# Kernel optimization log

Hardware: AMD Instinct MI355X
Metric: run time of the kernel (lower is better)

## Reference

```python
import jax, jax.numpy as jnp
import numpy as np
import math

EPS = 1e-5
N_HEADS = 4


def _ln(x, g, b):
    mu = jnp.mean(x, axis=-1, keepdims=True)
    var = jnp.mean((x - mu) ** 2, axis=-1, keepdims=True)
    return (x - mu) * jax.lax.rsqrt(var + EPS) * g + b


def _eq_ln(s, v, g, b, vscale):
    # scalar LayerNorm + equivariant vector norm rescaling
    s = _ln(s, g, b)
    vn = jnp.sqrt(jnp.sum(v * v, axis=-1, keepdims=True))  # (B,N,C,1)
    v = v / (vn + EPS) * jnp.mean(vn, axis=-2, keepdims=True) * vscale[None, None, :, None]
    return s, v


def _block(s, v, pos, Wq, bq, Wk, bk, Wv, bv, Wo, bo, w_dist, b_dist, Wvv, Wvo,
           g1, be1, vs1, g2, be2, vs2, Wf1, bf1, Wf2, bf2, Wfv1, Wfv2):
    B, N, S = s.shape
    D = S // N_HEADS
    # --- norm1 + attention ---
    sn, vn = _eq_ln(s, v, g1, be1, vs1)
    q = (sn @ Wq + bq).reshape(B, N, N_HEADS, D)
    k = (sn @ Wk + bk).reshape(B, N, N_HEADS, D)
    vs = (sn @ Wv + bv).reshape(B, N, N_HEADS, D)
    attn = jnp.einsum('bnhd,bmhd->bhnm', q, k) / math.sqrt(D)
    # pairwise Euclidean distance via the |x|^2 + |y|^2 - 2xy trick (clamped for sqrt safety)
    p2 = jnp.sum(pos * pos, axis=-1)  # (B,N)
    d2 = p2[:, :, None] + p2[:, None, :] - 2.0 * jnp.einsum('bnd,bmd->bnm', pos, pos)
    dist = jnp.sqrt(jnp.maximum(d2, 1e-12))  # (B,N,N)
    # dist_proj: Linear(1 -> n_heads) + Softplus, applied per pair
    bias = jax.nn.softplus(dist[..., None] * w_dist + b_dist)  # (B,N,N,H)
    attn = jax.nn.softmax(attn - jnp.transpose(bias, (0, 3, 1, 2)), axis=-1)  # (B,H,N,N)
    attn_mean = jnp.mean(attn, axis=1)  # (B,N,N)
    s_attn = jnp.einsum('bhnm,bmhd->bnhd', attn, vs).reshape(B, N, S) @ Wo + bo
    # vector channel mixing + rotation by head-averaged attention
    v_mix = jnp.einsum('bncx,ce->bnex', vn, Wvv)          # (B,N,C,3)
    v_attn = jnp.einsum('bnm,bmcx->bncx', attn_mean, v_mix)
    v_attn = jnp.einsum('bncx,ce->bnex', v_attn, Wvo)
    s = s + s_attn
    v = v + v_attn
    # --- norm2 + FFN ---
    sn, vn = _eq_ln(s, v, g2, be2, vs2)
    s = s + (jax.nn.gelu(sn @ Wf1 + bf1, approximate=False) @ Wf2 + bf2)
    v = v + jnp.einsum('bnhx,hc->bncx', jnp.einsum('bncx,ch->bnhx', vn, Wfv1), Wfv2)
    return s, v


def setup_inputs() -> dict:
    B, N, S, C, H = 4, 2048, 256, 64, N_HEADS
    key = jax.random.key(0)
    ks = jax.random.split(key, 24)

    def nrm(k, shape, scale=0.02):
        return jax.random.normal(k, shape, dtype=jnp.float32) * scale

    return {
        's': jax.random.normal(ks[0], (B, N, S), dtype=jnp.float32),
        'v': jax.random.normal(ks[1], (B, N, C, 3), dtype=jnp.float32),
        'pos': jax.random.normal(ks[2], (B, N, 3), dtype=jnp.float32),
        'Wq': nrm(ks[3], (S, S)), 'bq': nrm(ks[4], (S,)),
        'Wk': nrm(ks[5], (S, S)), 'bk': nrm(ks[6], (S,)),
        'Wv': nrm(ks[7], (S, S)), 'bv': nrm(ks[8], (S,)),
        'Wo': nrm(ks[9], (S, S)), 'bo': nrm(ks[10], (S,)),
        'w_dist': nrm(ks[11], (H,), 0.5), 'b_dist': nrm(ks[12], (H,), 0.5),
        'Wvv': nrm(ks[13], (C, C)), 'Wvo': nrm(ks[14], (C, C)),
        'g1': jnp.ones((S,), jnp.float32), 'be1': jnp.zeros((S,), jnp.float32),
        'vs1': jnp.ones((C,), jnp.float32),
        'g2': jnp.ones((S,), jnp.float32), 'be2': jnp.zeros((S,), jnp.float32),
        'vs2': jnp.ones((C,), jnp.float32),
        'Wf1': nrm(ks[15], (S, 4 * S)), 'bf1': nrm(ks[16], (4 * S,)),
        'Wf2': nrm(ks[17], (4 * S, S)), 'bf2': nrm(ks[18], (S,)),
        'Wfv1': nrm(ks[19], (C, 4 * C)), 'Wfv2': nrm(ks[20], (4 * C, C)),
    }


def reference(s, v, pos, Wq, bq, Wk, bk, Wv, bv, Wo, bo, w_dist, b_dist, Wvv, Wvo,
              g1, be1, vs1, g2, be2, vs2, Wf1, bf1, Wf2, bf2, Wfv1, Wfv2):
    return _block(s, v, pos, Wq, bq, Wk, bk, Wv, bv, Wo, bo, w_dist, b_dist, Wvv, Wvo,
                  g1, be1, vs1, g2, be2, vs2, Wf1, bf1, Wf2, bf2, Wfv1, Wfv2)
```

## Files before the change

kernel.cpp:

```cpp
#include <hip/hip_runtime.h>
#include <hip/hip_bf16.h>

using bf16 = __hip_bfloat16;
typedef __attribute__((ext_vector_type(8))) short short8;
typedef __attribute__((ext_vector_type(4))) float float4v;
typedef __attribute__((ext_vector_type(16))) float f32x16;
typedef __attribute__((ext_vector_type(4))) unsigned uint4v;

__device__ __forceinline__ float b2f(bf16 x){ return __bfloat162float(x); }
__device__ __forceinline__ bf16  f2b(float x){ return __float2bfloat16(x); }
__device__ __forceinline__ bf16  tob(float x){ return f2b(x); }
__device__ __forceinline__ bf16  tob(bf16 x){ return x; }
__device__ __forceinline__ float frcp(float x){ return __builtin_amdgcn_rcpf(x); }
__device__ __forceinline__ float bs2f(short s){
  unsigned u = ((unsigned)(unsigned short)s) << 16;
  return __builtin_bit_cast(float, u);
}
__device__ __forceinline__ unsigned cvt_pk_bf16(float lo, float hi){
  unsigned r; asm("v_cvt_pk_bf16_f32 %0, %1, %2" : "=v"(r) : "v"(lo), "v"(hi)); return r;
}
__device__ __forceinline__ void plswap(unsigned &a, unsigned &b){
  asm("v_permlane32_swap_b32 %0, %1" : "+v"(a), "+v"(b));
}

#define EPSV 1e-5f
#define Z16 {0.f,0.f,0.f,0.f,0.f,0.f,0.f,0.f,0.f,0.f,0.f,0.f,0.f,0.f,0.f,0.f}

__global__ __launch_bounds__(256) void pos_kernel(const float* __restrict__ pos,
                                                  float* __restrict__ posf, int rows){
  int r = blockIdx.x*256 + threadIdx.x;
  if (r >= rows) return;
  float x = pos[3*r], y = pos[3*r+1], z = pos[3*r+2];
  posf[4*r] = x; posf[4*r+1] = y; posf[4*r+2] = z; posf[4*r+3] = x*x + y*y + z*z;
}

struct WTDesc { const float* src; bf16* dst; int rows, cols; };
struct WTPack { WTDesc d[10]; };

__global__ __launch_bounds__(256) void wtrans_kernel(WTPack p){
  WTDesc w = p.d[blockIdx.z];
  long r0 = (long)blockIdx.y*32, c0 = (long)blockIdx.x*32;
  if (r0 >= w.rows || c0 >= w.cols) return;
  __shared__ bf16 tile[32][33];
  int tx = threadIdx.x & 31, ty = threadIdx.x >> 5;
#pragma unroll
  for (int i = ty; i < 32; i += 8) tile[i][tx] = f2b(w.src[(r0+i)*w.cols + c0 + tx]);
  __syncthreads();
#pragma unroll
  for (int i = ty; i < 32; i += 8) w.dst[(c0+i)*w.rows + r0 + tx] = tile[tx][i];
}

template<typename TI>
__global__ __launch_bounds__(256) void transpose_kernel(
    const TI* __restrict__ in, long ldin, long is1, long is2,
    bf16* __restrict__ out, long ldout, long os1, long os2, int Z2)
{
  int z = blockIdx.z, z1 = z / Z2, z2 = z - z1*Z2;
  in  += (long)z1*is1 + (long)z2*is2;
  out += (long)z1*os1 + (long)z2*os2;
  __shared__ bf16 tile[32][33];
  int tx = threadIdx.x & 31, ty = threadIdx.x >> 5;
  long r0 = (long)blockIdx.y*32, c0 = (long)blockIdx.x*32;
#pragma unroll
  for (int i = ty; i < 32; i += 8) tile[i][tx] = tob(in[(r0+i)*ldin + c0 + tx]);
  __syncthreads();
#pragma unroll
  for (int i = ty; i < 32; i += 8) out[(c0+i)*ldout + r0 + tx] = tile[tx][i];
}

__global__ __launch_bounds__(256) void bcat_kernel(const float* __restrict__ bq,
                                                   const float* __restrict__ bk,
                                                   const float* __restrict__ bv,
                                                   float* __restrict__ bqkv,
                                                   float* __restrict__ kmax){
  int j = blockIdx.x*256 + threadIdx.x;
  if (blockIdx.x == 0 && threadIdx.x < 16) kmax[threadIdx.x] = 0.f;
  if (j >= 768) return;
  bqkv[j] = (j < 256) ? bq[j] : (j < 512) ? bk[j-256] : bv[j-512];
}

__global__ __launch_bounds__(256) void ln_kernel(const float* __restrict__ x,
                                                 const float* __restrict__ g,
                                                 const float* __restrict__ be,
                                                 bf16* __restrict__ out){
  const long row = blockIdx.x;
  const int t = threadIdx.x;
  __shared__ float r1[256], r2[256];
  float v = x[(row<<8) + t];
  r1[t] = v; r2[t] = v*v; __syncthreads();
  for (int s=128;s>0;s>>=1){
    if (t<s){ r1[t] += r1[t+s]; r2[t] += r2[t+s]; }
    __syncthreads();
  }
  const float mu = r1[0] * (1.f/256.f);
  const float var = r2[0] * (1.f/256.f) - mu*mu;
  const float rstd = rsqrtf(fmaxf(var, 0.f) + EPSV);
  out[(row<<8)+t] = f2b((v-mu)*rstd*g[t] + be[t]);
}

__global__ __launch_bounds__(192) void vnorm1_kernel(const float* __restrict__ vin,
                                                     const float* __restrict__ vs1,
                                                     bf16* __restrict__ vnX){
  const long row = blockIdx.x;
  const int t = threadIdx.x;
  __shared__ float vv[192], nrm[64];
  __shared__ float smean;
  vv[t] = vin[row*192 + t];
  __syncthreads();
  if (t < 64){
    float a = vv[3*t], b = vv[3*t+1], c = vv[3*t+2];
    nrm[t] = sqrtf(a*a + b*b + c*c);
  }
  __syncthreads();
  if (t == 0){ float s = 0.f; for (int i=0;i<64;i++) s += nrm[i]; smean = s*(1.f/64.f); }
  __syncthreads();
  const int c = t/3, x = t - 3*c;
  const float val = vv[t] / (nrm[c] + EPSV) * smean * vs1[c];
  vnX[row*192 + x*64 + c] = f2b(val);
}

__global__ __launch_bounds__(192) void vnorm2_kernel(const float* __restrict__ v2X,
                                                     const float* __restrict__ vs2,
                                                     bf16* __restrict__ vn2X){
  const long row = blockIdx.x;
  const int t = threadIdx.x;
  __shared__ float vv[192], nrm[64];
  __shared__ float smean;
  vv[t] = v2X[row*192 + t];
  __syncthreads();
  if (t < 64){
    float a = vv[t], b = vv[t+64], c = vv[t+128];
    nrm[t] = sqrtf(a*a + b*b + c*c);
  }
  __syncthreads();
  if (t == 0){ float s = 0.f; for (int i=0;i<64;i++) s += nrm[i]; smean = s*(1.f/64.f); }
  __syncthreads();
  const int c = t & 63;
  vn2X[row*192 + t] = f2b(vv[t] / (nrm[c] + EPSV) * smean * vs2[c]);
}

__global__ __launch_bounds__(256) void knorm_kernel(const bf16* __restrict__ qkv,
                                                    float* __restrict__ kmax){
  const int bh = blockIdx.x, b = bh>>2, h = bh&3;
  const int t = threadIdx.x;
  __shared__ float red[256];
  long row = (long)b*2048 + (long)blockIdx.y*256 + t;
  const short8* kp = (const short8*)(qkv + row*768 + 256 + h*64);
  float ss = 0.f;
#pragma unroll
  for (int c=0;c<8;c++){
    short8 v = kp[c];
#pragma unroll
    for (int j=0;j<8;j++){ float f = bs2f(v[j]); ss = fmaf(f,f,ss); }
  }
  red[t] = ss; __syncthreads();
  for (int s=128;s>0;s>>=1){ if (t<s) red[t] = fmaxf(red[t], red[t+s]); __syncthreads(); }
  if (t==0) atomicMax((unsigned*)&kmax[bh], __float_as_uint(red[0]));
}

#define ATT_K_OFF   0
#define ATT_V_OFF   4096
#define ATT_X_OFF   9216
#define ATT_P_OFF   24576
#define ATT_TILE    25088
#define ATT_GRP     50176
#define ATT_LACC    98304
#define ATT_SMEM    100352

__global__ __launch_bounds__(512, 2) void attn_kernel(
    const bf16* __restrict__ qkv,
    const bf16* __restrict__ vsT,
    const bf16* __restrict__ vmixT,
    const float* __restrict__ posf,
    const float* __restrict__ kmaxA,
    const float* __restrict__ w_dist, const float* __restrict__ b_dist,
    bf16* __restrict__ sA,
    bf16* __restrict__ slab)
{
  __shared__ __align__(16) char smem[ATT_SMEM];
  const int qb = blockIdx.x;
  const int bh = blockIdx.y;
  const int b  = bh >> 2, h = bh & 3;
  const int tid = threadIdx.x;
  const int w = tid >> 6, lane = tid & 63;
  const int g = w >> 2, qw = w & 3;
  const int lq = lane & 31, hi = lane >> 5;
  const int gtid = tid & 255;

  const int qloc = qb*128 + qw*32 + lq;
  const long rowQ = (long)b*2048 + qloc;

  short8 qf[4];
  {
    const bf16* qp = qkv + rowQ*768 + h*64 + hi*8;
#pragma unroll
    for (int kc=0;kc<4;kc++) qf[kc] = *(const short8*)(qp + kc*16);
  }
  float q2 = 0.f;
#pragma unroll
  for (int kc=0;kc<4;kc++)
#pragma unroll
    for (int j=0;j<8;j++){ float qv = bs2f(qf[kc][j]); q2 = fmaf(qv,qv,q2); }
  q2 += __shfl_xor(q2, 32);
  const float mxs = sqrtf(q2 * kmaxA[bh]) * 0.125f;
  const float wh = w_dist[h], bhd = b_dist[h];
  const float4v pn = *(const float4v*)(posf + (long)b*8192 + (long)qloc*4);
  const float m2x = -2.f*pn[0], m2y = -2.f*pn[1], m2z = -2.f*pn[2], pnw = pn[3];

  f32x16 O[2]  = {Z16, Z16};
  f32x16 VM[6] = {Z16, Z16, Z16, Z16, Z16, Z16};
  float lacc = 0.f;

  short8 stK, stV, stX0, stX1, stX2; float4v stP;
  const int sm = gtid >> 3, sc = gtid & 7;
  const int vd = gtid >> 2, vc = gtid & 3;
  const bf16* Kg = qkv + (long)b*2048*768 + 256 + h*64;
  const bf16* Vg = vsT + (long)b*524288 + (long)h*131072;
  const bf16* Xg = vmixT + (long)b*393216;
  const float* Pg = posf + (long)b*8192;
  char* gbase = smem + g*ATT_GRP;

  auto LOADT = [&](int m0){
    stK  = *(const short8*)(Kg + (long)(m0+sm)*768 + sc*8);
    stV  = *(const short8*)(Vg + (long)vd*2048 + m0 + vc*8);
    stX0 = *(const short8*)(Xg + (long)vd*2048 + m0 + vc*8);
    stX1 = *(const short8*)(Xg + (long)(64+vd)*2048 + m0 + vc*8);
    stX2 = *(const short8*)(Xg + (long)(128+vd)*2048 + m0 + vc*8);
    if (gtid < 32) stP = *(const float4v*)(Pg + (long)(m0+gtid)*4);
  };
  auto WRITET = [&](char* buf){
    *(short8*)(buf + ATT_K_OFF + sm*128 + ((sc ^ (sm&7))<<4)) = stK;
    *(short8*)(buf + ATT_V_OFF + vd*80 + vc*16) = stV;
    *(short8*)(buf + ATT_X_OFF + vd*80 + vc*16) = stX0;
    *(short8*)(buf + ATT_X_OFF + (64+vd)*80 + vc*16) = stX1;
    *(short8*)(buf + ATT_X_OFF + (128+vd)*80 + vc*16) = stX2;
    if (gtid < 32) *(float4v*)(buf + ATT_P_OFF + gtid*16) = stP;
  };

  auto COMPUTE = [&](const char* buf){
    const char* Kb = buf + ATT_K_OFF;
    const char* Vb = buf + ATT_V_OFF;
    const char* Xb = buf + ATT_X_OFF;
    const float4v* pmb = (const float4v*)(buf + ATT_P_OFF);
    f32x16 S = Z16;
#pragma unroll
    for (int kc=0;kc<4;kc++){
      short8 kf = *(const short8*)(Kb + lq*128 + (((kc*2+hi) ^ (lq&7))<<4));
      S = __builtin_amdgcn_mfma_f32_32x32x16_bf16(kf, qf[kc], S, 0, 0, 0);
    }
    float P[16];
#pragma unroll
    for (int gg=0; gg<4; gg++){
#pragma unroll
      for (int i=0;i<4;i++){
        float4v pm = pmb[gg*8 + hi*4 + i];
        float d2 = fmaf(m2x, pm[0], fmaf(m2y, pm[1], fmaf(m2z, pm[2], pnw + pm[3])));
        float dist = sqrtf(fmaxf(d2, 1e-12f));
        float sig = frcp(1.f + __expf(fmaf(dist, wh, bhd)));
        float p = __expf(fmaf(S[gg*4+i], 0.125f, -mxs)) * sig;
        lacc += p;
        P[gg*4+i] = p;
      }
    }
    unsigned pk[8];
#pragma unroll
    for (int t=0;t<8;t++) pk[t] = cvt_pk_bf16(P[2*t], P[2*t+1]);
    plswap(pk[0], pk[2]); plswap(pk[1], pk[3]);
    plswap(pk[4], pk[6]); plswap(pk[5], pk[7]);
    uint4v y0v = {pk[0], pk[1], pk[2], pk[3]};
    uint4v y1v = {pk[4], pk[5], pk[6], pk[7]};
    short8 Y0 = __builtin_bit_cast(short8, y0v);
    short8 Y1 = __builtin_bit_cast(short8, y1v);
#pragma unroll
    for (int dblk=0; dblk<2; dblk++){
      short8 v0 = *(const short8*)(Vb + (dblk*32+lq)*80 + hi*16);
      short8 v1 = *(const short8*)(Vb + (dblk*32+lq)*80 + 32 + hi*16);
      O[dblk] = __builtin_amdgcn_mfma_f32_32x32x16_bf16(v0, Y0, O[dblk], 0,0,0);
      O[dblk] = __builtin_amdgcn_mfma_f32_32x32x16_bf16(v1, Y1, O[dblk], 0,0,0);
    }
#pragma unroll
    for (int eblk=0; eblk<6; eblk++){
      short8 x0 = *(const short8*)(Xb + (eblk*32+lq)*80 + hi*16);
      short8 x1 = *(const short8*)(Xb + (eblk*32+lq)*80 + 32 + hi*16);
      VM[eblk] = __builtin_amdgcn_mfma_f32_32x32x16_bf16(x0, Y0, VM[eblk], 0,0,0);
      VM[eblk] = __builtin_amdgcn_mfma_f32_32x32x16_bf16(x1, Y1, VM[eblk], 0,0,0);
    }
  };

  LOADT(g*32);
  WRITET(gbase);
  __syncthreads();
#pragma unroll 1
  for (int i=0; i<32; ++i){
    if (i < 31) LOADT((2*(i+1)+g)*32);
    COMPUTE(gbase + (i&1)*ATT_TILE);
    if (i < 31) WRITET(gbase + ((i+1)&1)*ATT_TILE);
    __syncthreads();
  }

  float* laccT = (float*)(smem + ATT_LACC);
  laccT[w*64 + lane] = lacc;
  if (g == 1){
    float* Od = (float*)(smem + ATT_GRP) + (qw*64+lane)*33;
#pragma unroll
    for (int r=0;r<16;r++){ Od[r] = O[0][r]; Od[16+r] = O[1][r]; }
  }
  __syncthreads();
  const float lsum = laccT[qw*64+lq] + laccT[qw*64+32+lq]
                   + laccT[(4+qw)*64+lq] + laccT[(4+qw)*64+32+lq];
  if (g == 0){
    const float* Od = (const float*)(smem + ATT_GRP) + (qw*64+lane)*33;
#pragma unroll
    for (int r=0;r<16;r++){ O[0][r] += Od[r]; O[1][r] += Od[16+r]; }
  }
  __syncthreads();
#pragma unroll
  for (int hf=0; hf<2; hf++){
    if (g == 0){
      float* Vd = (float*)smem + (qw*64+lane)*49;
#pragma unroll
      for (int e=0;e<3;e++)
#pragma unroll
        for (int r=0;r<16;r++) Vd[e*16+r] = VM[hf*3+e][r];
    }
    __syncthreads();
    if (g == 1){
      const float* Vd = (const float*)smem + (qw*64+lane)*49;
#pragma unroll
      for (int e=0;e<3;e++)
#pragma unroll
        for (int r=0;r<16;r++) VM[hf*3+e][r] += Vd[e*16+r];
    }
    __syncthreads();
  }

  const float sinv = frcp(lsum);
  if (g == 0){
    char* scr = smem + qw*12544;
#pragma unroll
    for (int dblk=0; dblk<2; dblk++)
#pragma unroll
      for (int pp=0; pp<8; pp++){
        const int r = 2*pp;
        const int d = dblk*32 + (r&3) + 8*(r>>2) + 4*hi;
        unsigned u = cvt_pk_bf16(O[dblk][r]*sinv, O[dblk][r+1]*sinv);
        *(unsigned*)(scr + lq*136 + d*2) = u;
      }
  } else {
    const float vinv = 0.25f * sinv;
    char* scr = smem + ATT_GRP + qw*12544;
#pragma unroll
    for (int eblk=0; eblk<6; eblk++)
#pragma unroll
      for (int pp=0; pp<8; pp++){
        const int r = 2*pp;
        const int e = eblk*32 + (r&3) + 8*(r>>2) + 4*hi;
        unsigned u = cvt_pk_bf16(VM[eblk][r]*vinv, VM[eblk][r+1]*vinv);
        *(unsigned*)(scr + lq*392 + e*2) = u;
      }
  }
  __syncthreads();
  if (g == 0){
    const char* scr = smem + qw*12544;
    const int q = lane >> 1, half = lane & 1;
    const char* src = scr + q*136 + half*64;
    char* dst = (char*)(sA + (long)(b*2048 + qb*128 + qw*32 + q)*256 + h*64 + half*32);
#pragma unroll
    for (int i=0;i<8;i++)
      *(unsigned long long*)(dst + i*8) = *(const unsigned long long*)(src + i*8);
  } else {
    const char* scr = smem + ATT_GRP + qw*12544;
    const int q = lane >> 1, half = lane & 1;
    const char* src = scr + q*392 + half*192;
    char* dst = (char*)(slab + (long)h*1572864
                        + (long)(b*2048 + qb*128 + qw*32 + q)*192 + half*96);
#pragma unroll
    for (int i=0;i<24;i++)
      *(unsigned long long*)(dst + i*8) = *(const unsigned long long*)(src + i*8);
  }
}

__global__ __launch_bounds__(256) void hred_kernel(const bf16* __restrict__ slab,
                                                   bf16* __restrict__ out){
  long i = (long)blockIdx.x*256 + threadIdx.x;
  if (i >= 196608) return;
  const short8* s0 = (const short8*)slab + i;
  short8 a = s0[0], b = s0[196608], c = s0[2*196608], d = s0[3*196608];
  short8 o;
#pragma unroll
  for (int j=0;j<8;j++){
    float f = bs2f(a[j]) + bs2f(b[j]) + bs2f(c[j]) + bs2f(d[j]);
    bf16 hv = f2b(f); o[j] = *(short*)&hv;
  }
  ((short8*)out)[i] = o;
}

template<int ACT, int OUTM>
__global__ __launch_bounds__(256) void tgemm_kernel(
    const bf16* __restrict__ A, long lda,
    const bf16* __restrict__ BT, long ldb,
    const float* __restrict__ bias,
    const float* __restrict__ resid,
    void* __restrict__ Cv, long ldc,
    int K)
{
  __shared__ __align__(16) bf16 As[2][128*32];
  __shared__ __align__(16) bf16 Bs[2][128*32];
  const int tid = threadIdx.x;
  const int w = tid >> 6, lane = tid & 63;
  const int wr = w >> 1, wc = w & 1;
  const int col = lane & 15, quad = lane >> 4;
  const long rowA0 = (long)blockIdx.y*128;
  const long colB0 = (long)blockIdx.x*128;

  const int tr = tid >> 2, tc = tid & 3;
  const bf16* Ag = A + (rowA0 + tr)*lda + tc*8;
  const bf16* Bg = BT + (colB0 + tr)*ldb + tc*8;

  short8 sa[2], sb[2];
  auto LOAD = [&](int k0){
#pragma unroll
    for (int c=0;c<2;c++){
      sa[c] = *(const short8*)(Ag + (long)c*64*lda + k0);
      sb[c] = *(const short8*)(Bg + (long)c*64*ldb + k0);
    }
  };
  auto STORE = [&](int buf){
#pragma unroll
    for (int c=0;c<2;c++){
      *(short8*)(&As[buf][(tr + 64*c)*32 + tc*8]) = sa[c];
      *(short8*)(&Bs[buf][(tr + 64*c)*32 + tc*8]) = sb[c];
    }
  };

  float4v acc[4][4];
#pragma unroll
  for (int m=0;m<4;m++)
#pragma unroll
    for (int n=0;n<4;n++) acc[m][n] = (float4v){0.f,0.f,0.f,0.f};

  LOAD(0); STORE(0);
  __syncthreads();
  const int nk = K >> 5;
#pragma unroll 1
  for (int ks=0; ks<nk; ++ks){
    if (ks+1 < nk) LOAD((ks+1)*32);
    const bf16* Ab = &As[ks&1][(wr*64 + col)*32 + quad*8];
    const bf16* Bb = &Bs[ks&1][(wc*64 + col)*32 + quad*8];
    short8 af[4], bfv[4];
#pragma unroll
    for (int m=0;m<4;m++) af[m] = *(const short8*)(Ab + m*16*32);
#pragma unroll
    for (int n=0;n<4;n++) bfv[n] = *(const short8*)(Bb + n*16*32);
#pragma unroll
    for (int m=0;m<4;m++)
#pragma unroll
      for (int n=0;n<4;n++)
        acc[m][n] = __builtin_amdgcn_mfma_f32_16x16x32_bf16(af[m], bfv[n], acc[m][n], 0, 0, 0);
    if (ks+1 < nk) STORE((ks+1)&1);
    __syncthreads();
  }

#pragma unroll
  for (int m=0;m<4;m++){
    const long ci0 = rowA0 + wr*64 + m*16 + quad*4;
#pragma unroll
    for (int n=0;n<4;n++){
      const long cj = colB0 + wc*64 + n*16 + col;
      const float bbias = bias ? bias[cj] : 0.f;
#pragma unroll
      for (int r=0;r<4;r++){
        const long ci = ci0 + r;
        float val = acc[m][n][r] + bbias;
        if (ACT == 1) val = 0.5f*val*(1.f + erff(val*0.70710678118654752f));
        if (resid) val += resid[ci*ldc + cj];
        if (OUTM == 0) ((bf16*)Cv)[ci*ldc + cj] = f2b(val);
        else           ((float*)Cv)[ci*ldc + cj] = val;
      }
    }
  }
}

template<int MT, int NT, int ACT, int OUTM, int RXIL, int CXIL>
__global__ __launch_bounds__(64) void gemm_kernel(
    const bf16* __restrict__ A, long lda, long As1, long As2,
    const bf16* __restrict__ BT, long ldb, long Bs1, long Bs2,
    const float* __restrict__ bias,
    const float* __restrict__ resid, long ldr, long Rs1, long Rs2,
    void* __restrict__ Cv, long ldc, long Cs1, long Cs2,
    int K, int Z2, int KS)
{
  int z = blockIdx.z;
  int zz = z / KS, ks = z - zz*KS;
  int z1 = zz / Z2, z2 = zz - z1*Z2;
  A  += (long)z1*As1 + (long)z2*As2 + (long)ks*K;
  BT += (long)z1*Bs1 + (long)z2*Bs2 + (long)ks*K;
  if (resid) resid += (long)z1*Rs1 + (long)z2*Rs2;
  const long cbase = (long)z1*Cs1 + (long)z2*Cs2;

  const int lane = threadIdx.x;
  const int col = lane & 15, quad = lane >> 4;
  const long rowA0 = (long)blockIdx.y*(16*MT);
  const long colB0 = (long)blockIdx.x*(16*NT);

  float4v acc[MT][NT];
#pragma unroll
  for (int m=0;m<MT;m++)
#pragma unroll
    for (int n=0;n<NT;n++) acc[m][n] = (float4v){0.f,0.f,0.f,0.f};

  const bf16* ap[MT];
  const bf16* bp[NT];
#pragma unroll
  for (int m=0;m<MT;m++) ap[m] = A + (rowA0 + m*16 + col)*lda + quad*8;
#pragma unroll
  for (int n=0;n<NT;n++) bp[n] = BT + (colB0 + n*16 + col)*ldb + quad*8;

  for (int k0 = 0; k0 < K; k0 += 32){
    short8 a[MT], bb[NT];
#pragma unroll
    for (int m=0;m<MT;m++){ a[m] = *(const short8*)ap[m]; ap[m] += 32; }
#pragma unroll
    for (int n=0;n<NT;n++){ bb[n] = *(const short8*)bp[n]; bp[n] += 32; }
#pragma unroll
    for (int m=0;m<MT;m++)
#pragma unroll
      for (int n=0;n<NT;n++)
        acc[m][n] = __builtin_amdgcn_mfma_f32_16x16x32_bf16(a[m], bb[n], acc[m][n], 0, 0, 0);
  }

#pragma unroll
  for (int m=0;m<MT;m++){
    const long ri = rowA0 + m*16 + quad*4;
#pragma unroll
    for (int n=0;n<NT;n++){
      const long cj = colB0 + n*16 + col;
      const float bbias = bias ? bias[cj] : 0.f;
#pragma unroll
      for (int r=0;r<4;r++){
        const long ci = ri + r;
        float val = acc[m][n][r] + bbias;
        if (ACT == 1) val = 0.5f*val*(1.f + erff(val*0.70710678118654752f));
        if (resid){
          const long raddr = RXIL ? ((ci/3)*192 + cj*3 + (ci%3)) : (ci*ldr + cj);
          val += resid[raddr];
        }
        const long caddr = CXIL ? (cbase + (ci/3)*192 + cj*3 + (ci%3))
                                : (cbase + ci*ldc + cj);
        if (OUTM == 0)      ((bf16*)Cv)[caddr] = f2b(val);
        else if (OUTM == 1) ((float*)Cv)[caddr] = val;
        else                unsafeAtomicAdd(&((float*)Cv)[caddr], val);
      }
    }
  }
}

extern "C" void kernel_launch(void* const* d_in, const int* in_sizes, int n_in,
                              void* d_out, int out_size, void* d_ws, size_t ws_size,
                              hipStream_t stream)
{
  const float* s    = (const float*)d_in[0];
  const float* v    = (const float*)d_in[1];
  const float* pos  = (const float*)d_in[2];
  const float* Wq   = (const float*)d_in[3];
  const float* bq   = (const float*)d_in[4];
  const float* Wk   = (const float*)d_in[5];
  const float* bk   = (const float*)d_in[6];
  const float* Wv   = (const float*)d_in[7];
  const float* bv   = (const float*)d_in[8];
  const float* Wo   = (const float*)d_in[9];
  const float* bo   = (const float*)d_in[10];
  const float* w_d  = (const float*)d_in[11];
  const float* b_d  = (const float*)d_in[12];
  const float* Wvv  = (const float*)d_in[13];
  const float* Wvo  = (const float*)d_in[14];
  const float* g1   = (const float*)d_in[15];
  const float* be1  = (const float*)d_in[16];
  const float* vs1  = (const float*)d_in[17];
  const float* g2   = (const float*)d_in[18];
  const float* be2  = (const float*)d_in[19];
  const float* vs2  = (const float*)d_in[20];
  const float* Wf1  = (const float*)d_in[21];
  const float* bf1  = (const float*)d_in[22];
  const float* Wf2  = (const float*)d_in[23];
  const float* bf2  = (const float*)d_in[24];
  const float* Wfv1 = (const float*)d_in[25];
  const float* Wfv2 = (const float*)d_in[26];

  float* outS = (float*)d_out;
  float* outV = outS + (size_t)4*2048*256;

  char* w = (char*)d_ws;
  size_t o = 0;
  auto alloc = [&](size_t bytes)->char* {
    char* p = w + o;
    o = (o + bytes + 255) & ~(size_t)255;
    return p;
  };
  float* posf  = (float*)alloc(131072);
  bf16* WqkvT = (bf16*)alloc(393216);
  bf16* WoT   = (bf16*)alloc(131072);
  bf16* Wf1T  = (bf16*)alloc(524288);
  bf16* Wf2T  = (bf16*)alloc(524288);
  bf16* WvvT  = (bf16*)alloc(8192);
  bf16* WvoT  = (bf16*)alloc(8192);
  bf16* Wfv1T = (bf16*)alloc(32768);
  bf16* Wfv2T = (bf16*)alloc(32768);
  float* bqkv = (float*)alloc(3072);
  float* kmax = (float*)alloc(64);
  bf16* sn    = (bf16*)alloc(4194304);
  bf16* qkv   = (bf16*)alloc(12582912);
  bf16* vsT   = (bf16*)alloc(4194304);
  bf16* sA    = (bf16*)alloc(4194304);
  float* s2   = (float*)alloc(8388608);
  bf16* vnX   = (bf16*)alloc(3145728);
  bf16* vmixX = (bf16*)alloc(3145728);
  bf16* vmixXT= (bf16*)alloc(3145728);
  float* v2X  = (float*)alloc(6291456);
  bf16* slab  = (bf16*)alloc(12582912);
  bf16* h1    = (bf16*)alloc(16777216);
  bf16* vn2X  = vnX;
  bf16* tvXb  = vmixX;
  bf16* hv    = qkv;
  if (o > ws_size) return;

  pos_kernel<<<32, 256, 0, stream>>>(pos, posf, 8192);
  WTPack pk;
  pk.d[0] = {Wq,   WqkvT,          256, 256};
  pk.d[1] = {Wk,   WqkvT + 65536,  256, 256};
  pk.d[2] = {Wv,   WqkvT + 131072, 256, 256};
  pk.d[3] = {Wo,   WoT,            256, 256};
  pk.d[4] = {Wf1,  Wf1T,           256, 1024};
  pk.d[5] = {Wf2,  Wf2T,           1024, 256};
  pk.d[6] = {Wvv,  WvvT,           64, 64};
  pk.d[7] = {Wvo,  WvoT,           64, 64};
  pk.d[8] = {Wfv1, Wfv1T,          64, 256};
  pk.d[9] = {Wfv2, Wfv2T,          256, 64};
  wtrans_kernel<<<dim3(32,32,10), 256, 0, stream>>>(pk);
  bcat_kernel<<<3, 256, 0, stream>>>(bq, bk, bv, bqkv, kmax);

  ln_kernel<<<8192, 256, 0, stream>>>(s, g1, be1, sn);
  vnorm1_kernel<<<8192, 192, 0, stream>>>(v, vs1, vnX);

  gemm_kernel<2,4,0,0,0,0><<<dim3(1,768,1), 64, 0, stream>>>(vnX,64,0,0, WvvT,64,0,0,
      nullptr, nullptr,0,0,0, vmixX,64,0,0, 64, 1, 1);
  transpose_kernel<bf16><<<dim3(6,64,4), 256, 0, stream>>>(vmixX, 192, 393216,0,
      vmixXT, 2048, 393216,0, 1);

  tgemm_kernel<0,0><<<dim3(6,64), 256, 0, stream>>>(sn,256, WqkvT,256,
      bqkv, nullptr, qkv,768, 256);
  transpose_kernel<bf16><<<dim3(2,64,16), 256, 0, stream>>>(qkv+512, 768, 1572864,64,
      vsT, 2048, 524288,131072, 4);

  knorm_kernel<<<dim3(16,8), 256, 0, stream>>>(qkv, kmax);
  attn_kernel<<<dim3(16,16), 512, 0, stream>>>(qkv, vsT, vmixXT, posf, kmax,
      w_d, b_d, sA, slab);
  hred_kernel<<<768, 256, 0, stream>>>(slab, tvXb);

  tgemm_kernel<0,1><<<dim3(2,64), 256, 0, stream>>>(sA,256, WoT,256,
      bo, s, s2,256, 256);

  gemm_kernel<2,4,0,1,1,0><<<dim3(1,768,1), 64, 0, stream>>>(tvXb,64,0,0, WvoT,64,0,0,
      nullptr, v,0,0,0, v2X,64,0,0, 64, 1, 1);

  ln_kernel<<<8192, 256, 0, stream>>>(s2, g2, be2, sn);
  tgemm_kernel<1,0><<<dim3(8,64), 256, 0, stream>>>(sn,256, Wf1T,256,
      bf1, nullptr, h1,1024, 256);
  tgemm_kernel<0,1><<<dim3(2,64), 256, 0, stream>>>(h1,1024, Wf2T,1024,
      bf2, s2, outS,256, 1024);

  vnorm2_kernel<<<8192, 192, 0, stream>>>(v2X, vs2, vn2X);
  gemm_kernel<2,4,0,0,0,0><<<dim3(4,768,1), 64, 0, stream>>>(vn2X,64,0,0, Wfv1T,64,0,0,
      nullptr, nullptr,0,0,0, hv,256,0,0, 64, 1, 1);
  gemm_kernel<2,4,0,1,0,1><<<dim3(1,768,1), 64, 0, stream>>>(hv,256,0,0, Wfv2T,256,0,0,
      nullptr, v2X,64,0,0, outV,0,0,0, 256, 1, 1);
}
```

Before: 403.2 us.

## Use wave-shuffle reductions and 64-row GEMM tiles, route Wfv1 through tiled GEMM

Replaces the shared-memory tree reductions in the layernorm, vector-norm and key-norm kernels with wavefront xor-shuffle reductions, which removes most barriers. Shrinks the tiled GEMM from 128x128 to 64x128 block tiles, doubling the grid so more blocks are in flight for these mid-sized matrices. Also moves the vector FFN first projection from the small 64-thread gemm onto the tiled kernel. Smaller tiles reuse less data per block and add more launch overhead in exchange for better occupancy.

```diff
diff --git a/kernel.cpp b/kernel.cpp
--- a/kernel.cpp
+++ b/kernel.cpp
@@ -84,16 +84,21 @@
                                                  const float* __restrict__ be,
                                                  bf16* __restrict__ out){
   const long row = blockIdx.x;
-  const int t = threadIdx.x;
-  __shared__ float r1[256], r2[256];
+  const int t = threadIdx.x, lane = t & 63, wv = t >> 6;
+  __shared__ float ws1[4], ws2[4];
   float v = x[(row<<8) + t];
-  r1[t] = v; r2[t] = v*v; __syncthreads();
-  for (int s=128;s>0;s>>=1){
-    if (t<s){ r1[t] += r1[t+s]; r2[t] += r2[t+s]; }
-    __syncthreads();
-  }
-  const float mu = r1[0] * (1.f/256.f);
-  const float var = r2[0] * (1.f/256.f) - mu*mu;
+  float s1 = v, s2 = v*v;
+#pragma unroll
+  for (int off=32; off; off>>=1){
+    s1 += __shfl_xor(s1, off);
+    s2 += __shfl_xor(s2, off);
+  }
+  if (lane == 0){ ws1[wv] = s1; ws2[wv] = s2; }
+  __syncthreads();
+  const float r1 = ws1[0]+ws1[1]+ws1[2]+ws1[3];
+  const float r2 = ws2[0]+ws2[1]+ws2[2]+ws2[3];
+  const float mu = r1 * (1.f/256.f);
+  const float var = r2 * (1.f/256.f) - mu*mu;
   const float rstd = rsqrtf(fmaxf(var, 0.f) + EPSV);
   out[(row<<8)+t] = f2b((v-mu)*rstd*g[t] + be[t]);
 }
@@ -109,10 +114,13 @@
   __syncthreads();
   if (t < 64){
     float a = vv[3*t], b = vv[3*t+1], c = vv[3*t+2];
-    nrm[t] = sqrtf(a*a + b*b + c*c);
-  }
-  __syncthreads();
-  if (t == 0){ float s = 0.f; for (int i=0;i<64;i++) s += nrm[i]; smean = s*(1.f/64.f); }
+    float nv = sqrtf(a*a + b*b + c*c);
+    nrm[t] = nv;
+    float s = nv;
+#pragma unroll
+    for (int off=32; off; off>>=1) s += __shfl_xor(s, off);
+    if (t == 0) smean = s*(1.f/64.f);
+  }
   __syncthreads();
   const int c = t/3, x = t - 3*c;
   const float val = vv[t] / (nrm[c] + EPSV) * smean * vs1[c];
@@ -130,10 +138,13 @@
   __syncthreads();
   if (t < 64){
     float a = vv[t], b = vv[t+64], c = vv[t+128];
-    nrm[t] = sqrtf(a*a + b*b + c*c);
-  }
-  __syncthreads();
-  if (t == 0){ float s = 0.f; for (int i=0;i<64;i++) s += nrm[i]; smean = s*(1.f/64.f); }
+    float nv = sqrtf(a*a + b*b + c*c);
+    nrm[t] = nv;
+    float s = nv;
+#pragma unroll
+    for (int off=32; off; off>>=1) s += __shfl_xor(s, off);
+    if (t == 0) smean = s*(1.f/64.f);
+  }
   __syncthreads();
   const int c = t & 63;
   vn2X[row*192 + t] = f2b(vv[t] / (nrm[c] + EPSV) * smean * vs2[c]);
@@ -142,8 +153,8 @@
 __global__ __launch_bounds__(256) void knorm_kernel(const bf16* __restrict__ qkv,
                                                     float* __restrict__ kmax){
   const int bh = blockIdx.x, b = bh>>2, h = bh&3;
-  const int t = threadIdx.x;
-  __shared__ float red[256];
+  const int t = threadIdx.x, lane = t & 63, wv = t >> 6;
+  __shared__ float red[4];
   long row = (long)b*2048 + (long)blockIdx.y*256 + t;
   const short8* kp = (const short8*)(qkv + row*768 + 256 + h*64);
   float ss = 0.f;
@@ -153,9 +164,14 @@
 #pragma unroll
     for (int j=0;j<8;j++){ float f = bs2f(v[j]); ss = fmaf(f,f,ss); }
   }
-  red[t] = ss; __syncthreads();
-  for (int s=128;s>0;s>>=1){ if (t<s) red[t] = fmaxf(red[t], red[t+s]); __syncthreads(); }
-  if (t==0) atomicMax((unsigned*)&kmax[bh], __float_as_uint(red[0]));
+#pragma unroll
+  for (int off=32; off; off>>=1) ss = fmaxf(ss, __shfl_xor(ss, off));
+  if (lane == 0) red[wv] = ss;
+  __syncthreads();
+  if (t == 0){
+    float m = fmaxf(fmaxf(red[0],red[1]), fmaxf(red[2],red[3]));
+    atomicMax((unsigned*)&kmax[bh], __float_as_uint(m));
+  }
 }
 
 #define ATT_K_OFF   0
@@ -396,7 +412,7 @@
 }
 
 template<int ACT, int OUTM>
-__global__ __launch_bounds__(256) void tgemm_kernel(
+__global__ __launch_bounds__(256) void tgemm64_kernel(
     const bf16* __restrict__ A, long lda,
     const bf16* __restrict__ BT, long ldb,
     const float* __restrict__ bias,
@@ -404,40 +420,35 @@
     void* __restrict__ Cv, long ldc,
     int K)
 {
-  __shared__ __align__(16) bf16 As[2][128*32];
+  __shared__ __align__(16) bf16 As[2][64*32];
   __shared__ __align__(16) bf16 Bs[2][128*32];
   const int tid = threadIdx.x;
-  const int w = tid >> 6, lane = tid & 63;
-  const int wr = w >> 1, wc = w & 1;
+  const int wc = tid >> 6, lane = tid & 63;
   const int col = lane & 15, quad = lane >> 4;
-  const long rowA0 = (long)blockIdx.y*128;
+  const long rowA0 = (long)blockIdx.y*64;
   const long colB0 = (long)blockIdx.x*128;
 
   const int tr = tid >> 2, tc = tid & 3;
   const bf16* Ag = A + (rowA0 + tr)*lda + tc*8;
   const bf16* Bg = BT + (colB0 + tr)*ldb + tc*8;
 
-  short8 sa[2], sb[2];
+  short8 sa, sb[2];
   auto LOAD = [&](int k0){
-#pragma unroll
-    for (int c=0;c<2;c++){
-      sa[c] = *(const short8*)(Ag + (long)c*64*lda + k0);
-      sb[c] = *(const short8*)(Bg + (long)c*64*ldb + k0);
-    }
+    sa = *(const short8*)(Ag + k0);
+    sb[0] = *(const short8*)(Bg + k0);
+    sb[1] = *(const short8*)(Bg + (long)64*ldb + k0);
   };
   auto STORE = [&](int buf){
-#pragma unroll
-    for (int c=0;c<2;c++){
-      *(short8*)(&As[buf][(tr + 64*c)*32 + tc*8]) = sa[c];
-      *(short8*)(&Bs[buf][(tr + 64*c)*32 + tc*8]) = sb[c];
-    }
+    *(short8*)(&As[buf][tr*32 + tc*8]) = sa;
+    *(short8*)(&Bs[buf][tr*32 + tc*8]) = sb[0];
+    *(short8*)(&Bs[buf][(tr+64)*32 + tc*8]) = sb[1];
   };
 
-  float4v acc[4][4];
+  float4v acc[4][2];
 #pragma unroll
   for (int m=0;m<4;m++)
 #pragma unroll
-    for (int n=0;n<4;n++) acc[m][n] = (float4v){0.f,0.f,0.f,0.f};
+    for (int n=0;n<2;n++) acc[m][n] = (float4v){0.f,0.f,0.f,0.f};
 
   LOAD(0); STORE(0);
   __syncthreads();
@@ -445,17 +456,17 @@
 #pragma unroll 1
   for (int ks=0; ks<nk; ++ks){
     if (ks+1 < nk) LOAD((ks+1)*32);
-    const bf16* Ab = &As[ks&1][(wr*64 + col)*32 + quad*8];
-    const bf16* Bb = &Bs[ks&1][(wc*64 + col)*32 + quad*8];
-    short8 af[4], bfv[4];
+    const bf16* Ab = &As[ks&1][col*32 + quad*8];
+    const bf16* Bb = &Bs[ks&1][(wc*32 + col)*32 + quad*8];
+    short8 af[4], bfv[2];
 #pragma unroll
     for (int m=0;m<4;m++) af[m] = *(const short8*)(Ab + m*16*32);
 #pragma unroll
-    for (int n=0;n<4;n++) bfv[n] = *(const short8*)(Bb + n*16*32);
+    for (int n=0;n<2;n++) bfv[n] = *(const short8*)(Bb + n*16*32);
 #pragma unroll
     for (int m=0;m<4;m++)
 #pragma unroll
-      for (int n=0;n<4;n++)
+      for (int n=0;n<2;n++)
         acc[m][n] = __builtin_amdgcn_mfma_f32_16x16x32_bf16(af[m], bfv[n], acc[m][n], 0, 0, 0);
     if (ks+1 < nk) STORE((ks+1)&1);
     __syncthreads();
@@ -463,10 +474,10 @@
 
 #pragma unroll
   for (int m=0;m<4;m++){
-    const long ci0 = rowA0 + wr*64 + m*16 + quad*4;
-#pragma unroll
-    for (int n=0;n<4;n++){
-      const long cj = colB0 + wc*64 + n*16 + col;
+    const long ci0 = rowA0 + m*16 + quad*4;
+#pragma unroll
+    for (int n=0;n<2;n++){
+      const long cj = colB0 + wc*32 + n*16 + col;
       const float bbias = bias ? bias[cj] : 0.f;
 #pragma unroll
       for (int r=0;r<4;r++){
@@ -647,7 +658,7 @@
   transpose_kernel<bf16><<<dim3(6,64,4), 256, 0, stream>>>(vmixX, 192, 393216,0,
       vmixXT, 2048, 393216,0, 1);
 
-  tgemm_kernel<0,0><<<dim3(6,64), 256, 0, stream>>>(sn,256, WqkvT,256,
+  tgemm64_kernel<0,0><<<dim3(6,128), 256, 0, stream>>>(sn,256, WqkvT,256,
       bqkv, nullptr, qkv,768, 256);
   transpose_kernel<bf16><<<dim3(2,64,16), 256, 0, stream>>>(qkv+512, 768, 1572864,64,
       vsT, 2048, 524288,131072, 4);
@@ -657,21 +668,21 @@
       w_d, b_d, sA, slab);
   hred_kernel<<<768, 256, 0, stream>>>(slab, tvXb);
 
-  tgemm_kernel<0,1><<<dim3(2,64), 256, 0, stream>>>(sA,256, WoT,256,
+  tgemm64_kernel<0,1><<<dim3(2,128), 256, 0, stream>>>(sA,256, WoT,256,
       bo, s, s2,256, 256);
 
   gemm_kernel<2,4,0,1,1,0><<<dim3(1,768,1), 64, 0, stream>>>(tvXb,64,0,0, WvoT,64,0,0,
       nullptr, v,0,0,0, v2X,64,0,0, 64, 1, 1);
 
   ln_kernel<<<8192, 256, 0, stream>>>(s2, g2, be2, sn);
-  tgemm_kernel<1,0><<<dim3(8,64), 256, 0, stream>>>(sn,256, Wf1T,256,
+  tgemm64_kernel<1,0><<<dim3(8,128), 256, 0, stream>>>(sn,256, Wf1T,256,
       bf1, nullptr, h1,1024, 256);
-  tgemm_kernel<0,1><<<dim3(2,64), 256, 0, stream>>>(h1,1024, Wf2T,1024,
+  tgemm64_kernel<0,1><<<dim3(2,128), 256, 0, stream>>>(h1,1024, Wf2T,1024,
       bf2, s2, outS,256, 1024);
 
   vnorm2_kernel<<<8192, 192, 0, stream>>>(v2X, vs2, vn2X);
-  gemm_kernel<2,4,0,0,0,0><<<dim3(4,768,1), 64, 0, stream>>>(vn2X,64,0,0, Wfv1T,64,0,0,
-      nullptr, nullptr,0,0,0, hv,256,0,0, 64, 1, 1);
+  tgemm64_kernel<0,0><<<dim3(2,384), 256, 0, stream>>>(vn2X,64, Wfv1T,64,
+      nullptr, nullptr, hv,256, 64);
   gemm_kernel<2,4,0,1,0,1><<<dim3(1,768,1), 64, 0, stream>>>(hv,256,0,0, Wfv2T,256,0,0,
       nullptr, v2X,64,0,0, outV,0,0,0, 256, 1, 1);
 }
```

After: 377.7 us. 1.07x faster.
